# Kernel tuning notes

Hardware: AMD Instinct MI355X
Metric: run time of the kernel (lower is better)

The kernel has to match this reference:

```python
import jax, jax.numpy as jnp
import numpy as np

N = 50000      # nodes
E = 600000     # edges
F_IN = 128     # num_node_features
H = 128        # hidden_channels
C = 10         # num_classes
G = 128        # graphs in batch


def setup_inputs() -> dict:
    key = jax.random.key(0)
    ks = jax.random.split(key, 12)
    x = jax.random.normal(ks[0], (N, F_IN), dtype=jnp.float32)
    edge_index = jax.random.randint(ks[1], (2, E), 0, N, dtype=jnp.int64)
    batch = jnp.sort(jax.random.randint(ks[2], (N,), 0, G, dtype=jnp.int64))
    s = 0.05
    return {
        "x": x,
        "W1": jax.random.normal(ks[3], (F_IN, H), jnp.float32) * s,
        "b1": jnp.zeros((H,), jnp.float32),
        "W2": jax.random.normal(ks[4], (H, H), jnp.float32) * s,
        "b2": jnp.zeros((H,), jnp.float32),
        "W3": jax.random.normal(ks[5], (H, H), jnp.float32) * s,
        "b3": jnp.zeros((H,), jnp.float32),
        "Wl": jax.random.normal(ks[6], (H, C), jnp.float32) * s,
        "bl": jnp.zeros((C,), jnp.float32),
        "edge_index": edge_index,
        "batch": batch,
    }


def _gcn_conv(h, W, b, src, dst, norm, n):
    # h: [N, din] -> linear (no bias), gather, scale, scatter-add, + bias
    h = h @ W                                  # [N, dout]
    msg = norm[:, None] * h[src]               # [E+N, dout]
    out = jax.ops.segment_sum(msg, dst, num_segments=n)
    return out + b


def reference(x, W1, b1, W2, b2, W3, b3, Wl, bl, edge_index, batch):
    n = x.shape[0]
    # add self-loops (PyG GCNConv default) and symmetric normalization
    loop = jnp.arange(n, dtype=edge_index.dtype)
    src = jnp.concatenate([edge_index[0], loop])   # [E+N]
    dst = jnp.concatenate([edge_index[1], loop])   # [E+N]
    deg = jax.ops.segment_sum(jnp.ones_like(dst, dtype=x.dtype), dst, num_segments=n)
    dinv = jnp.where(deg > 0, jax.lax.rsqrt(deg), 0.0)
    norm = dinv[src] * dinv[dst]                   # [E+N]

    h = jax.nn.relu(_gcn_conv(x, W1, b1, src, dst, norm, n))
    h = jax.nn.relu(_gcn_conv(h, W2, b2, src, dst, norm, n))
    h = jax.nn.relu(_gcn_conv(h, W3, b3, src, dst, norm, n))

    # global mean pool over graph ids
    sums = jax.ops.segment_sum(h, batch, num_segments=G)           # [G, H]
    cnts = jax.ops.segment_sum(jnp.ones((n,), h.dtype), batch, num_segments=G)
    pooled = sums / jnp.maximum(cnts, 1.0)[:, None]

    # dropout is identity at inference; final linear classifier
    return pooled @ Wl + bl                                        # [G, C]
```

## Files before the change

kernel.cpp:

```cpp
#include <hip/hip_runtime.h>

#define HID 128
#define CLS 10
#define RCAP 64

typedef short short8 __attribute__((ext_vector_type(8)));
typedef float f32x4 __attribute__((ext_vector_type(4)));

__device__ __forceinline__ unsigned short f2bf(float f) {
  union { float f; unsigned u; } v; v.f = f;
  unsigned u = v.u;
  return (unsigned short)((u + 0x7FFFu + ((u >> 16) & 1u)) >> 16);
}
__device__ __forceinline__ float bf_lo(unsigned p) { return __uint_as_float(p << 16); }
__device__ __forceinline__ float bf_hi(unsigned p) { return __uint_as_float(p & 0xFFFF0000u); }


__global__ __launch_bounds__(256) void zero_wt(int* __restrict__ degi, int n, int nbN,
                                               float* __restrict__ pooled, int gh,
                                               const float* __restrict__ W1,
                                               const float* __restrict__ W2,
                                               const float* __restrict__ W3,
                                               unsigned short* __restrict__ Wt,
                                               unsigned short* __restrict__ TbZeroRow) {
  int b = blockIdx.x;
  if (b < nbN) {
    int i = b * 256 + threadIdx.x;
    if (i < n) degi[i] = 0;
    if (i < gh) pooled[i] = 0.f;
    if (b == 0 && threadIdx.x < 16) {
      uint4 z; z.x = z.y = z.z = z.w = 0u;
      *(uint4*)&TbZeroRow[threadIdx.x * 8] = z;
    }
    return;
  }
  int wb = b - nbN;
  int mat = wb >> 4;
  int part = wb & 15;
  const float* W = (mat == 0) ? W1 : (mat == 1) ? W2 : W3;
  unsigned short* o = Wt + (size_t)mat * HID * HID;
  int base = part * (HID * HID / 16);
  for (int r = 0; r < HID * HID / 16; r += 256) {
    int idx = base + r + threadIdx.x;
    int k = idx >> 7, nn = idx & 127;
    o[nn * HID + k] = f2bf(W[idx]);
  }
}

__global__ __launch_bounds__(256) void degree_fill(const int* __restrict__ src,
                                                   const int* __restrict__ dst,
                                                   int* __restrict__ degi,
                                                   int* __restrict__ col_src, int E) {
  int e = blockIdx.x * 256 + threadIdx.x;
  if (e >= E) return;
  int d = dst[e];
  int slot = atomicAdd(&degi[d], 1);
  if (slot < RCAP) col_src[(size_t)d * RCAP + slot] = src[e];
}


#define WTP 136

__global__ __launch_bounds__(256) void gemm_mfma(const void* __restrict__ Aptr,
                                                 int a_fp32,
                                                 const unsigned short* __restrict__ Wt,
                                                 const int* __restrict__ degi,
                                                 unsigned short* __restrict__ Tb,
                                                 int* __restrict__ pad_col,
                                                 int nrows) {
  __shared__ unsigned short sW[HID][WTP];
  int tid = threadIdx.x;
  int wave = tid >> 6, lane = tid & 63;
  int m_lo = lane & 15, quad = lane >> 4;
  int row0 = blockIdx.x * 128;
  int rbase = row0 + wave * 32;

  uint4 araw[2][4];
#pragma unroll
  for (int tr = 0; tr < 2; ++tr) {
    int grow = rbase + tr * 16 + m_lo;
    int gr = (grow < nrows) ? grow : (nrows - 1);
    if (a_fp32) {
      const float* Arow = (const float*)Aptr + (size_t)gr * HID;
#pragma unroll
      for (int kb = 0; kb < 4; ++kb) {
        float4 f0 = *(const float4*)&Arow[kb * 32 + quad * 8];
        float4 f1 = *(const float4*)&Arow[kb * 32 + quad * 8 + 4];
        uint4 u;
        u.x = (unsigned)f2bf(f0.x) | ((unsigned)f2bf(f0.y) << 16);
        u.y = (unsigned)f2bf(f0.z) | ((unsigned)f2bf(f0.w) << 16);
        u.z = (unsigned)f2bf(f1.x) | ((unsigned)f2bf(f1.y) << 16);
        u.w = (unsigned)f2bf(f1.z) | ((unsigned)f2bf(f1.w) << 16);
        araw[tr][kb] = u;
      }
    } else {
      const uint4* Arow = (const uint4*)((const unsigned*)Aptr + (size_t)gr * 64);
#pragma unroll
      for (int kb = 0; kb < 4; ++kb) araw[tr][kb] = Arow[kb * 4 + quad];
    }
  }

  const uint4* Wt4 = (const uint4*)Wt;
#pragma unroll
  for (int i = 0; i < 8; ++i) {
    int idx = i * 256 + tid;
    *(uint4*)&sW[idx >> 4][(idx & 15) * 8] = Wt4[idx];
  }
  __syncthreads();

  f32x4 acc[2][8];
#pragma unroll
  for (int tr = 0; tr < 2; ++tr)
#pragma unroll
    for (int tc = 0; tc < 8; ++tc) acc[tr][tc] = (f32x4)(0.f);

#pragma unroll
  for (int kb = 0; kb < 4; ++kb) {
    short8 b[8];
#pragma unroll
    for (int tc = 0; tc < 8; ++tc) {
      union { uint4 u; short8 s; } cv;
      cv.u = *(const uint4*)&sW[tc * 16 + m_lo][kb * 32 + quad * 8];
      b[tc] = cv.s;
    }
#pragma unroll
    for (int tr = 0; tr < 2; ++tr) {
      union { uint4 u; short8 s; } av;
      av.u = araw[tr][kb];
#pragma unroll
      for (int tc = 0; tc < 8; ++tc)
        acc[tr][tc] = __builtin_amdgcn_mfma_f32_16x16x32_bf16(av.s, b[tc], acc[tr][tc], 0, 0, 0);
    }
  }

#pragma unroll
  for (int tr = 0; tr < 2; ++tr) {
#pragma unroll
    for (int r = 0; r < 4; ++r) {
      int grow = rbase + tr * 16 + quad * 4 + r;
      if (grow < nrows) {
        int dgv = degi[grow];
        float s = rsqrtf((float)dgv + 1.0f);
        unsigned short* orow = &Tb[(size_t)grow * HID];
#pragma unroll
        for (int tc = 0; tc < 8; ++tc)
          orow[tc * 16 + m_lo] = f2bf(s * acc[tr][tc][r]);
        if (pad_col && m_lo == 0) {
          int d = dgv < RCAP ? dgv : RCAP;
          int dp = (d + 3) & ~3;
          for (int sl = d; sl < dp; ++sl)
            pad_col[(size_t)grow * RCAP + sl] = nrows;
        }
      }
    }
  }
}


__device__ __forceinline__ void agg_node(const unsigned* __restrict__ Tb2,
                                         const int* __restrict__ degi,
                                         const int* __restrict__ col_src,
                                         const float* __restrict__ bias,
                                         int node, int l4, float a[8]) {
  uint4 sv = *(const uint4*)&Tb2[(size_t)node * 64 + l4 * 4];
  a[0] = bf_lo(sv.x); a[1] = bf_hi(sv.x); a[2] = bf_lo(sv.y); a[3] = bf_hi(sv.y);
  a[4] = bf_lo(sv.z); a[5] = bf_hi(sv.z); a[6] = bf_lo(sv.w); a[7] = bf_hi(sv.w);
  int deg = degi[node];
  int dc = deg < RCAP ? deg : RCAP;
  int dp = (dc + 3) & ~3;
  const int* row = &col_src[(size_t)node * RCAP];
  int j = 0;
  for (; j + 8 <= dp; j += 8) {
    int idx[8];
#pragma unroll
    for (int u = 0; u < 8; ++u) idx[u] = row[j + u];
    uint4 v[8];
#pragma unroll
    for (int u = 0; u < 8; ++u) v[u] = *(const uint4*)&Tb2[(size_t)idx[u] * 64 + l4 * 4];
#pragma unroll
    for (int u = 0; u < 8; ++u) {
      a[0] += bf_lo(v[u].x); a[1] += bf_hi(v[u].x);
      a[2] += bf_lo(v[u].y); a[3] += bf_hi(v[u].y);
      a[4] += bf_lo(v[u].z); a[5] += bf_hi(v[u].z);
      a[6] += bf_lo(v[u].w); a[7] += bf_hi(v[u].w);
    }
  }
  if (j < dp) {
    int idx[4];
#pragma unroll
    for (int u = 0; u < 4; ++u) idx[u] = row[j + u];
    uint4 v[4];
#pragma unroll
    for (int u = 0; u < 4; ++u) v[u] = *(const uint4*)&Tb2[(size_t)idx[u] * 64 + l4 * 4];
#pragma unroll
    for (int u = 0; u < 4; ++u) {
      a[0] += bf_lo(v[u].x); a[1] += bf_hi(v[u].x);
      a[2] += bf_lo(v[u].y); a[3] += bf_hi(v[u].y);
      a[4] += bf_lo(v[u].z); a[5] += bf_hi(v[u].z);
      a[6] += bf_lo(v[u].w); a[7] += bf_hi(v[u].w);
    }
  }
  float di = rsqrtf((float)deg + 1.0f);
  float4 bs0 = *(const float4*)&bias[l4 * 8];
  float4 bs1 = *(const float4*)&bias[l4 * 8 + 4];
  a[0] = fmaxf(di * a[0] + bs0.x, 0.f);
  a[1] = fmaxf(di * a[1] + bs0.y, 0.f);
  a[2] = fmaxf(di * a[2] + bs0.z, 0.f);
  a[3] = fmaxf(di * a[3] + bs0.w, 0.f);
  a[4] = fmaxf(di * a[4] + bs1.x, 0.f);
  a[5] = fmaxf(di * a[5] + bs1.y, 0.f);
  a[6] = fmaxf(di * a[6] + bs1.z, 0.f);
  a[7] = fmaxf(di * a[7] + bs1.w, 0.f);
}

__global__ __launch_bounds__(256) void aggregate(const unsigned* __restrict__ Tb2,
                                                 const int* __restrict__ degi,
                                                 const int* __restrict__ col_src,
                                                 const float* __restrict__ bias,
                                                 unsigned* __restrict__ Hb, int n) {
  int w = (blockIdx.x * 256 + threadIdx.x) >> 6;
  int lane = threadIdx.x & 63;
  int sub = lane >> 4;
  int l4 = lane & 15;
  int node = w * 4 + sub;
  if (node >= n) return;
  float a[8];
  agg_node(Tb2, degi, col_src, bias, node, l4, a);
  uint4 o;
  o.x = (unsigned)f2bf(a[0]) | ((unsigned)f2bf(a[1]) << 16);
  o.y = (unsigned)f2bf(a[2]) | ((unsigned)f2bf(a[3]) << 16);
  o.z = (unsigned)f2bf(a[4]) | ((unsigned)f2bf(a[5]) << 16);
  o.w = (unsigned)f2bf(a[6]) | ((unsigned)f2bf(a[7]) << 16);
  *(uint4*)&Hb[(size_t)node * 64 + l4 * 4] = o;
}

#define SPP 132

__global__ __launch_bounds__(256) void aggregate_pool(const unsigned* __restrict__ Tb2,
                                                      const int* __restrict__ degi,
                                                      const int* __restrict__ col_src,
                                                      const float* __restrict__ bias,
                                                      const int* __restrict__ batch,
                                                      float* __restrict__ pooled, int n) {
  __shared__ float sP[16][SPP];
  int tid = threadIdx.x;
  int wave = tid >> 6, lane = tid & 63;
  int sub = lane >> 4;
  int l4 = lane & 15;
  int base = blockIdx.x * 16;
  int nl = wave * 4 + sub;
  int node = base + nl;
  bool active = (node < n);

  float a[8] = {0.f, 0.f, 0.f, 0.f, 0.f, 0.f, 0.f, 0.f};
  if (active) agg_node(Tb2, degi, col_src, bias, node, l4, a);
  *(float4*)&sP[nl][l4 * 8] = make_float4(a[0], a[1], a[2], a[3]);
  *(float4*)&sP[nl][l4 * 8 + 4] = make_float4(a[4], a[5], a[6], a[7]);
  __syncthreads();

  if (tid < HID) {
    int g = -1;
    float acc = 0.f;
    for (int i = 0; i < 16; ++i) {
      int nd = base + i;
      if (nd >= n) break;
      int bi = batch[nd];
      if (bi != g) {
        if (g >= 0) atomicAdd(&pooled[g * HID + tid], acc);
        acc = 0.f;
        g = bi;
      }
      acc += sP[i][tid];
    }
    if (g >= 0) atomicAdd(&pooled[g * HID + tid], acc);
  }
}

__global__ __launch_bounds__(128) void classify_k(const float* __restrict__ pooled,
                                                  const int* __restrict__ batch,
                                                  const float* __restrict__ Wl,
                                                  const float* __restrict__ bl,
                                                  float* __restrict__ out, int n) {
  int g = blockIdx.x;
  int t = threadIdx.x;
  int lo = 0, hi = n;
  while (lo < hi) { int mid = (lo + hi) >> 1; if (batch[mid] < g) lo = mid + 1; else hi = mid; }
  int s = lo;
  hi = n;
  while (lo < hi) { int mid = (lo + hi) >> 1; if (batch[mid] < g + 1) lo = mid + 1; else hi = mid; }
  float c = fmaxf((float)(lo - s), 1.0f);
  __shared__ float p[HID];
  p[t] = pooled[g * HID + t] / c;
  __syncthreads();
  if (t < CLS) {
    float o = bl[t];
    for (int j = 0; j < HID; ++j) o += p[j] * Wl[j * CLS + t];
    out[g * CLS + t] = o;
  }
}


extern "C" void kernel_launch(void* const* d_in, const int* in_sizes, int n_in,
                              void* d_out, int out_size, void* d_ws, size_t ws_size,
                              hipStream_t stream) {
  const float* x  = (const float*)d_in[0];
  const float* W1 = (const float*)d_in[1];
  const float* b1 = (const float*)d_in[2];
  const float* W2 = (const float*)d_in[3];
  const float* b2 = (const float*)d_in[4];
  const float* W3 = (const float*)d_in[5];
  const float* b3 = (const float*)d_in[6];
  const float* Wl = (const float*)d_in[7];
  const float* bl = (const float*)d_in[8];
  const int* edge_index = (const int*)d_in[9];
  const int* batch = (const int*)d_in[10];

  const int N = in_sizes[10];
  const int E = in_sizes[9] / 2;
  const int G = out_size / CLS;
  const int* src = edge_index;
  const int* dst = edge_index + E;

  uintptr_t p = (uintptr_t)d_ws;
  auto take = [&](size_t bytes) -> void* {
    void* r = (void*)p;
    p += (bytes + 255) & ~(size_t)255;
    return r;
  };
  int*      degi      = (int*)take((size_t)N * 4);
  int*      col_src   = (int*)take((size_t)N * RCAP * 4);
  unsigned short* WtA = (unsigned short*)take((size_t)3 * HID * HID * 2);
  unsigned short* bufTb = (unsigned short*)take((size_t)(N + 1) * HID * 2);
  unsigned* bufHb     = (unsigned*)take((size_t)N * 64 * 4);
  float*    pooled    = (float*)take((size_t)G * HID * 4);

  int nbN = (N + 255) / 256;
  int nbE = (E + 255) / 256;

  zero_wt<<<nbN + 48, 256, 0, stream>>>(degi, N, nbN, pooled, G * HID, W1, W2, W3, WtA,
                                        bufTb + (size_t)N * HID);
  degree_fill<<<nbE, 256, 0, stream>>>(src, dst, degi, col_src, E);

  int gemmBlocks = (N + 127) / 128;
  int waves = (N + 3) / 4;
  int aggBlocks = (waves + 3) / 4;

  gemm_mfma<<<gemmBlocks, 256, 0, stream>>>(x, 1, WtA, degi, bufTb, col_src, N);
  aggregate<<<aggBlocks, 256, 0, stream>>>((unsigned*)bufTb, degi, col_src, b1, bufHb, N);
  gemm_mfma<<<gemmBlocks, 256, 0, stream>>>(bufHb, 0, WtA + (size_t)HID * HID, degi, bufTb,
                                            nullptr, N);
  aggregate<<<aggBlocks, 256, 0, stream>>>((unsigned*)bufTb, degi, col_src, b2, bufHb, N);
  gemm_mfma<<<gemmBlocks, 256, 0, stream>>>(bufHb, 0, WtA + (size_t)2 * HID * HID, degi, bufTb,
                                            nullptr, N);
  aggregate_pool<<<(N + 15) / 16, 256, 0, stream>>>((unsigned*)bufTb, degi, col_src, b3,
                                                    batch, pooled, N);
  classify_k<<<G, 128, 0, stream>>>(pooled, batch, Wl, bl, (float*)d_out, N);
}
```

Measured before the change: 247.3 us.

## Bucket neighbor lists by source-index range and aggregate four nodes per thread

Neighbor lists are split into four buckets by source node index range, each with its own count, so the gathers for one bucket touch a narrower part of the feature table and should hit cache better. Aggregation now processes four nodes per 16-lane group and interleaves the gathers of two nodes so more loads are in flight. Outputs use nontemporal stores, and the pooling kernel works on 64 nodes per block. The trade-offs are more padding slots, a per-bucket cap of 24 that could drop edges for skewed graphs, and more registers per thread.

```diff
diff --git a/kernel.cpp b/kernel.cpp
--- a/kernel.cpp
+++ b/kernel.cpp
@@ -2,7 +2,9 @@
 
 #define HID 128
 #define CLS 10
-#define RCAP 64
+#define NW 4
+#define BCAP 24
+#define NSTR (NW * BCAP)
 
 typedef short short8 __attribute__((ext_vector_type(8)));
 typedef float f32x4 __attribute__((ext_vector_type(4)));
@@ -16,7 +18,7 @@
 __device__ __forceinline__ float bf_hi(unsigned p) { return __uint_as_float(p & 0xFFFF0000u); }
 
 
-__global__ __launch_bounds__(256) void zero_wt(int* __restrict__ degi, int n, int nbN,
+__global__ __launch_bounds__(256) void zero_wt(int* __restrict__ degw, int n, int nbN,
                                                float* __restrict__ pooled, int gh,
                                                const float* __restrict__ W1,
                                                const float* __restrict__ W2,
@@ -26,7 +28,7 @@
   int b = blockIdx.x;
   if (b < nbN) {
     int i = b * 256 + threadIdx.x;
-    if (i < n) degi[i] = 0;
+    if (i < n) { int4 z4; z4.x = z4.y = z4.z = z4.w = 0; *(int4*)&degw[(size_t)i * 4] = z4; }
     if (i < gh) pooled[i] = 0.f;
     if (b == 0 && threadIdx.x < 16) {
       uint4 z; z.x = z.y = z.z = z.w = 0u;
@@ -49,13 +51,17 @@
 
 __global__ __launch_bounds__(256) void degree_fill(const int* __restrict__ src,
                                                    const int* __restrict__ dst,
-                                                   int* __restrict__ degi,
-                                                   int* __restrict__ col_src, int E) {
+                                                   int* __restrict__ degw,
+                                                   int* __restrict__ col_src, int E,
+                                                   float wscale) {
   int e = blockIdx.x * 256 + threadIdx.x;
   if (e >= E) return;
+  int s = src[e];
   int d = dst[e];
-  int slot = atomicAdd(&degi[d], 1);
-  if (slot < RCAP) col_src[(size_t)d * RCAP + slot] = src[e];
+  int w = (int)((float)s * wscale);
+  if (w > NW - 1) w = NW - 1;
+  int slot = atomicAdd(&degw[(size_t)d * 4 + w], 1);
+  if (slot < BCAP) col_src[(size_t)d * NSTR + w * BCAP + slot] = s;
 }
 
 
@@ -64,7 +70,7 @@
 __global__ __launch_bounds__(256) void gemm_mfma(const void* __restrict__ Aptr,
                                                  int a_fp32,
                                                  const unsigned short* __restrict__ Wt,
-                                                 const int* __restrict__ degi,
+                                                 const int* __restrict__ degw,
                                                  unsigned short* __restrict__ Tb,
                                                  int* __restrict__ pad_col,
                                                  int nrows) {
@@ -139,17 +145,22 @@
     for (int r = 0; r < 4; ++r) {
       int grow = rbase + tr * 16 + quad * 4 + r;
       if (grow < nrows) {
-        int dgv = degi[grow];
+        int4 cwv = *(const int4*)&degw[(size_t)grow * 4];
+        int dgv = cwv.x + cwv.y + cwv.z + cwv.w;
         float s = rsqrtf((float)dgv + 1.0f);
         unsigned short* orow = &Tb[(size_t)grow * HID];
 #pragma unroll
         for (int tc = 0; tc < 8; ++tc)
           orow[tc * 16 + m_lo] = f2bf(s * acc[tr][tc][r]);
         if (pad_col && m_lo == 0) {
-          int d = dgv < RCAP ? dgv : RCAP;
-          int dp = (d + 3) & ~3;
-          for (int sl = d; sl < dp; ++sl)
-            pad_col[(size_t)grow * RCAP + sl] = nrows;
+#pragma unroll
+          for (int w = 0; w < NW; ++w) {
+            int cc = (w == 0) ? cwv.x : (w == 1) ? cwv.y : (w == 2) ? cwv.z : cwv.w;
+            int d = cc < BCAP ? cc : BCAP;
+            int dp = (d + 3) & ~3;
+            for (int sl = d; sl < dp; ++sl)
+              pad_col[(size_t)grow * NSTR + w * BCAP + sl] = nrows;
+          }
         }
       }
     }
@@ -157,122 +168,180 @@
 }
 
 
-__device__ __forceinline__ void agg_node(const unsigned* __restrict__ Tb2,
-                                         const int* __restrict__ degi,
+__device__ __forceinline__ void accum_row(float a[8], uint4 v) {
+  a[0] += bf_lo(v.x); a[1] += bf_hi(v.x);
+  a[2] += bf_lo(v.y); a[3] += bf_hi(v.y);
+  a[4] += bf_lo(v.z); a[5] += bf_hi(v.z);
+  a[6] += bf_lo(v.w); a[7] += bf_hi(v.w);
+}
+
+__device__ __forceinline__ uint4 tb_row(const unsigned* __restrict__ Tb2, int idx, int l4) {
+  return *(const uint4*)&Tb2[(size_t)idx * 64 + l4 * 4];
+}
+
+__device__ __forceinline__ int cw_get(int4 v, int w) {
+  return (w == 0) ? v.x : (w == 1) ? v.y : (w == 2) ? v.z : v.w;
+}
+
+__device__ __forceinline__ void agg_quad(const unsigned* __restrict__ Tb2,
                                          const int* __restrict__ col_src,
-                                         const float* __restrict__ bias,
-                                         int node, int l4, float a[8]) {
-  uint4 sv = *(const uint4*)&Tb2[(size_t)node * 64 + l4 * 4];
-  a[0] = bf_lo(sv.x); a[1] = bf_hi(sv.x); a[2] = bf_lo(sv.y); a[3] = bf_hi(sv.y);
-  a[4] = bf_lo(sv.z); a[5] = bf_hi(sv.z); a[6] = bf_lo(sv.w); a[7] = bf_hi(sv.w);
-  int deg = degi[node];
-  int dc = deg < RCAP ? deg : RCAP;
-  int dp = (dc + 3) & ~3;
-  const int* row = &col_src[(size_t)node * RCAP];
-  int j = 0;
-  for (; j + 8 <= dp; j += 8) {
-    int idx[8];
-#pragma unroll
-    for (int u = 0; u < 8; ++u) idx[u] = row[j + u];
-    uint4 v[8];
-#pragma unroll
-    for (int u = 0; u < 8; ++u) v[u] = *(const uint4*)&Tb2[(size_t)idx[u] * 64 + l4 * 4];
-#pragma unroll
-    for (int u = 0; u < 8; ++u) {
-      a[0] += bf_lo(v[u].x); a[1] += bf_hi(v[u].x);
-      a[2] += bf_lo(v[u].y); a[3] += bf_hi(v[u].y);
-      a[4] += bf_lo(v[u].z); a[5] += bf_hi(v[u].z);
-      a[6] += bf_lo(v[u].w); a[7] += bf_hi(v[u].w);
-    }
-  }
-  if (j < dp) {
-    int idx[4];
-#pragma unroll
-    for (int u = 0; u < 4; ++u) idx[u] = row[j + u];
-    uint4 v[4];
-#pragma unroll
-    for (int u = 0; u < 4; ++u) v[u] = *(const uint4*)&Tb2[(size_t)idx[u] * 64 + l4 * 4];
-#pragma unroll
-    for (int u = 0; u < 4; ++u) {
-      a[0] += bf_lo(v[u].x); a[1] += bf_hi(v[u].x);
-      a[2] += bf_lo(v[u].y); a[3] += bf_hi(v[u].y);
-      a[4] += bf_lo(v[u].z); a[5] += bf_hi(v[u].z);
-      a[6] += bf_lo(v[u].w); a[7] += bf_hi(v[u].w);
-    }
-  }
-  float di = rsqrtf((float)deg + 1.0f);
+                                         const int4 cw[4], const int nd[4], int l4,
+                                         int nzero, float acc[4][8]) {
+#pragma unroll
+  for (int c = 0; c < 4; ++c) {
+    uint4 sv = tb_row(Tb2, nd[c], l4);
+    acc[c][0] = bf_lo(sv.x); acc[c][1] = bf_hi(sv.x);
+    acc[c][2] = bf_lo(sv.y); acc[c][3] = bf_hi(sv.y);
+    acc[c][4] = bf_lo(sv.z); acc[c][5] = bf_hi(sv.z);
+    acc[c][6] = bf_lo(sv.w); acc[c][7] = bf_hi(sv.w);
+  }
+#pragma unroll
+  for (int w = 0; w < NW; ++w) {
+#pragma unroll
+    for (int cp = 0; cp < 2; ++cp) {
+      const int c0 = cp * 2, c1 = cp * 2 + 1;
+      int n0 = cw_get(cw[c0], w); n0 = n0 < BCAP ? n0 : BCAP;
+      int n1 = cw_get(cw[c1], w); n1 = n1 < BCAP ? n1 : BCAP;
+      int dp0 = (n0 + 3) & ~3, dp1 = (n1 + 3) & ~3;
+      const int* r0 = &col_src[(size_t)nd[c0] * NSTR + w * BCAP];
+      const int* r1 = &col_src[(size_t)nd[c1] * NSTR + w * BCAP];
+      int4 i0 = (dp0 > 0) ? *(const int4*)r0 : make_int4(nzero, nzero, nzero, nzero);
+      int4 i1 = (dp1 > 0) ? *(const int4*)r1 : make_int4(nzero, nzero, nzero, nzero);
+      uint4 v0[4], v1[4];
+      v0[0] = tb_row(Tb2, i0.x, l4); v0[1] = tb_row(Tb2, i0.y, l4);
+      v0[2] = tb_row(Tb2, i0.z, l4); v0[3] = tb_row(Tb2, i0.w, l4);
+      v1[0] = tb_row(Tb2, i1.x, l4); v1[1] = tb_row(Tb2, i1.y, l4);
+      v1[2] = tb_row(Tb2, i1.z, l4); v1[3] = tb_row(Tb2, i1.w, l4);
+#pragma unroll
+      for (int u = 0; u < 4; ++u) accum_row(acc[c0], v0[u]);
+#pragma unroll
+      for (int u = 0; u < 4; ++u) accum_row(acc[c1], v1[u]);
+      for (int j = 4; j < dp0; j += 4) {
+        int4 ii = *(const int4*)(r0 + j);
+        uint4 a0 = tb_row(Tb2, ii.x, l4), a1 = tb_row(Tb2, ii.y, l4);
+        uint4 a2 = tb_row(Tb2, ii.z, l4), a3 = tb_row(Tb2, ii.w, l4);
+        accum_row(acc[c0], a0); accum_row(acc[c0], a1);
+        accum_row(acc[c0], a2); accum_row(acc[c0], a3);
+      }
+      for (int j = 4; j < dp1; j += 4) {
+        int4 ii = *(const int4*)(r1 + j);
+        uint4 a0 = tb_row(Tb2, ii.x, l4), a1 = tb_row(Tb2, ii.y, l4);
+        uint4 a2 = tb_row(Tb2, ii.z, l4), a3 = tb_row(Tb2, ii.w, l4);
+        accum_row(acc[c1], a0); accum_row(acc[c1], a1);
+        accum_row(acc[c1], a2); accum_row(acc[c1], a3);
+      }
+    }
+  }
+}
+
+__global__ __launch_bounds__(256) void aggregate(const unsigned* __restrict__ Tb2,
+                                                 const int* __restrict__ degw,
+                                                 const int* __restrict__ col_src,
+                                                 const float* __restrict__ bias,
+                                                 unsigned* __restrict__ Hb, int n, int nzero) {
+  int tid = threadIdx.x;
+  int g = tid >> 4, l4 = tid & 15;
+  int base = blockIdx.x * 64 + g * 4;
+  int nd[4]; int4 cw[4];
+#pragma unroll
+  for (int c = 0; c < 4; ++c) {
+    int node = base + c;
+    nd[c] = node < n ? node : (n - 1);
+    cw[c] = *(const int4*)&degw[(size_t)nd[c] * 4];
+  }
+  float acc[4][8];
+  agg_quad(Tb2, col_src, cw, nd, l4, nzero, acc);
+
   float4 bs0 = *(const float4*)&bias[l4 * 8];
   float4 bs1 = *(const float4*)&bias[l4 * 8 + 4];
-  a[0] = fmaxf(di * a[0] + bs0.x, 0.f);
-  a[1] = fmaxf(di * a[1] + bs0.y, 0.f);
-  a[2] = fmaxf(di * a[2] + bs0.z, 0.f);
-  a[3] = fmaxf(di * a[3] + bs0.w, 0.f);
-  a[4] = fmaxf(di * a[4] + bs1.x, 0.f);
-  a[5] = fmaxf(di * a[5] + bs1.y, 0.f);
-  a[6] = fmaxf(di * a[6] + bs1.z, 0.f);
-  a[7] = fmaxf(di * a[7] + bs1.w, 0.f);
-}
-
-__global__ __launch_bounds__(256) void aggregate(const unsigned* __restrict__ Tb2,
-                                                 const int* __restrict__ degi,
-                                                 const int* __restrict__ col_src,
-                                                 const float* __restrict__ bias,
-                                                 unsigned* __restrict__ Hb, int n) {
-  int w = (blockIdx.x * 256 + threadIdx.x) >> 6;
-  int lane = threadIdx.x & 63;
-  int sub = lane >> 4;
-  int l4 = lane & 15;
-  int node = w * 4 + sub;
-  if (node >= n) return;
-  float a[8];
-  agg_node(Tb2, degi, col_src, bias, node, l4, a);
-  uint4 o;
-  o.x = (unsigned)f2bf(a[0]) | ((unsigned)f2bf(a[1]) << 16);
-  o.y = (unsigned)f2bf(a[2]) | ((unsigned)f2bf(a[3]) << 16);
-  o.z = (unsigned)f2bf(a[4]) | ((unsigned)f2bf(a[5]) << 16);
-  o.w = (unsigned)f2bf(a[6]) | ((unsigned)f2bf(a[7]) << 16);
-  *(uint4*)&Hb[(size_t)node * 64 + l4 * 4] = o;
+#pragma unroll
+  for (int c = 0; c < 4; ++c) {
+    int node = base + c;
+    if (node < n) {
+      int deg = cw[c].x + cw[c].y + cw[c].z + cw[c].w;
+      float di = rsqrtf((float)deg + 1.0f);
+      float o0 = fmaxf(di * acc[c][0] + bs0.x, 0.f);
+      float o1 = fmaxf(di * acc[c][1] + bs0.y, 0.f);
+      float o2 = fmaxf(di * acc[c][2] + bs0.z, 0.f);
+      float o3 = fmaxf(di * acc[c][3] + bs0.w, 0.f);
+      float o4 = fmaxf(di * acc[c][4] + bs1.x, 0.f);
+      float o5 = fmaxf(di * acc[c][5] + bs1.y, 0.f);
+      float o6 = fmaxf(di * acc[c][6] + bs1.z, 0.f);
+      float o7 = fmaxf(di * acc[c][7] + bs1.w, 0.f);
+      union { uint4 u4; unsigned long long ll[2]; } o;
+      o.u4.x = (unsigned)f2bf(o0) | ((unsigned)f2bf(o1) << 16);
+      o.u4.y = (unsigned)f2bf(o2) | ((unsigned)f2bf(o3) << 16);
+      o.u4.z = (unsigned)f2bf(o4) | ((unsigned)f2bf(o5) << 16);
+      o.u4.w = (unsigned)f2bf(o6) | ((unsigned)f2bf(o7) << 16);
+      unsigned long long* dst = (unsigned long long*)&Hb[(size_t)node * 64 + l4 * 4];
+      __builtin_nontemporal_store(o.ll[0], dst);
+      __builtin_nontemporal_store(o.ll[1], dst + 1);
+    }
+  }
 }
 
 #define SPP 132
 
 __global__ __launch_bounds__(256) void aggregate_pool(const unsigned* __restrict__ Tb2,
-                                                      const int* __restrict__ degi,
+                                                      const int* __restrict__ degw,
                                                       const int* __restrict__ col_src,
                                                       const float* __restrict__ bias,
                                                       const int* __restrict__ batch,
-                                                      float* __restrict__ pooled, int n) {
-  __shared__ float sP[16][SPP];
+                                                      float* __restrict__ pooled, int n,
+                                                      int nzero) {
+  __shared__ float sP[64][SPP];
   int tid = threadIdx.x;
-  int wave = tid >> 6, lane = tid & 63;
-  int sub = lane >> 4;
-  int l4 = lane & 15;
-  int base = blockIdx.x * 16;
-  int nl = wave * 4 + sub;
-  int node = base + nl;
-  bool active = (node < n);
-
-  float a[8] = {0.f, 0.f, 0.f, 0.f, 0.f, 0.f, 0.f, 0.f};
-  if (active) agg_node(Tb2, degi, col_src, bias, node, l4, a);
-  *(float4*)&sP[nl][l4 * 8] = make_float4(a[0], a[1], a[2], a[3]);
-  *(float4*)&sP[nl][l4 * 8 + 4] = make_float4(a[4], a[5], a[6], a[7]);
+  int g = tid >> 4, l4 = tid & 15;
+  int base = blockIdx.x * 64;
+  int nb = base + g * 4;
+  int nd[4]; int4 cw[4];
+#pragma unroll
+  for (int c = 0; c < 4; ++c) {
+    int node = nb + c;
+    nd[c] = node < n ? node : (n - 1);
+    cw[c] = *(const int4*)&degw[(size_t)nd[c] * 4];
+  }
+  float acc[4][8];
+  agg_quad(Tb2, col_src, cw, nd, l4, nzero, acc);
+
+  float4 bs0 = *(const float4*)&bias[l4 * 8];
+  float4 bs1 = *(const float4*)&bias[l4 * 8 + 4];
+#pragma unroll
+  for (int c = 0; c < 4; ++c) {
+    int deg = cw[c].x + cw[c].y + cw[c].z + cw[c].w;
+    float di = rsqrtf((float)deg + 1.0f);
+    float o0 = fmaxf(di * acc[c][0] + bs0.x, 0.f);
+    float o1 = fmaxf(di * acc[c][1] + bs0.y, 0.f);
+    float o2 = fmaxf(di * acc[c][2] + bs0.z, 0.f);
+    float o3 = fmaxf(di * acc[c][3] + bs0.w, 0.f);
+    float o4 = fmaxf(di * acc[c][4] + bs1.x, 0.f);
+    float o5 = fmaxf(di * acc[c][5] + bs1.y, 0.f);
+    float o6 = fmaxf(di * acc[c][6] + bs1.z, 0.f);
+    float o7 = fmaxf(di * acc[c][7] + bs1.w, 0.f);
+    int nl = g * 4 + c;
+    *(float4*)&sP[nl][l4 * 8] = make_float4(o0, o1, o2, o3);
+    *(float4*)&sP[nl][l4 * 8 + 4] = make_float4(o4, o5, o6, o7);
+  }
   __syncthreads();
 
-  if (tid < HID) {
-    int g = -1;
-    float acc = 0.f;
-    for (int i = 0; i < 16; ++i) {
-      int nd = base + i;
-      if (nd >= n) break;
-      int bi = batch[nd];
-      if (bi != g) {
-        if (g >= 0) atomicAdd(&pooled[g * HID + tid], acc);
-        acc = 0.f;
-        g = bi;
+  {
+    int f = tid & 127;
+    int h = tid >> 7;
+    int i0 = h * 32, i1 = i0 + 32;
+    int gq = -1;
+    float accv = 0.f;
+    for (int i = i0; i < i1; ++i) {
+      int ndl = base + i;
+      if (ndl >= n) break;
+      int bi = batch[ndl];
+      if (bi != gq) {
+        if (gq >= 0) atomicAdd(&pooled[gq * HID + f], accv);
+        accv = 0.f;
+        gq = bi;
       }
-      acc += sP[i][tid];
-    }
-    if (g >= 0) atomicAdd(&pooled[g * HID + tid], acc);
+      accv += sP[i][f];
+    }
+    if (gq >= 0) atomicAdd(&pooled[gq * HID + f], accv);
   }
 }
 
@@ -327,8 +396,8 @@
     p += (bytes + 255) & ~(size_t)255;
     return r;
   };
-  int*      degi      = (int*)take((size_t)N * 4);
-  int*      col_src   = (int*)take((size_t)N * RCAP * 4);
+  int*      degw      = (int*)take((size_t)N * 4 * 4);
+  int*      col_src   = (int*)take((size_t)N * NSTR * 4);
   unsigned short* WtA = (unsigned short*)take((size_t)3 * HID * HID * 2);
   unsigned short* bufTb = (unsigned short*)take((size_t)(N + 1) * HID * 2);
   unsigned* bufHb     = (unsigned*)take((size_t)N * 64 * 4);
@@ -336,23 +405,23 @@
 
   int nbN = (N + 255) / 256;
   int nbE = (E + 255) / 256;
-
-  zero_wt<<<nbN + 48, 256, 0, stream>>>(degi, N, nbN, pooled, G * HID, W1, W2, W3, WtA,
+  float wscale = (float)NW / (float)N;
+
+  zero_wt<<<nbN + 48, 256, 0, stream>>>(degw, N, nbN, pooled, G * HID, W1, W2, W3, WtA,
                                         bufTb + (size_t)N * HID);
-  degree_fill<<<nbE, 256, 0, stream>>>(src, dst, degi, col_src, E);
+  degree_fill<<<nbE, 256, 0, stream>>>(src, dst, degw, col_src, E, wscale);
 
   int gemmBlocks = (N + 127) / 128;
-  int waves = (N + 3) / 4;
-  int aggBlocks = (waves + 3) / 4;
-
-  gemm_mfma<<<gemmBlocks, 256, 0, stream>>>(x, 1, WtA, degi, bufTb, col_src, N);
-  aggregate<<<aggBlocks, 256, 0, stream>>>((unsigned*)bufTb, degi, col_src, b1, bufHb, N);
-  gemm_mfma<<<gemmBlocks, 256, 0, stream>>>(bufHb, 0, WtA + (size_t)HID * HID, degi, bufTb,
+  int aggBlocks = (N + 63) / 64;
+
+  gemm_mfma<<<gemmBlocks, 256, 0, stream>>>(x, 1, WtA, degw, bufTb, col_src, N);
+  aggregate<<<aggBlocks, 256, 0, stream>>>((unsigned*)bufTb, degw, col_src, b1, bufHb, N, N);
+  gemm_mfma<<<gemmBlocks, 256, 0, stream>>>(bufHb, 0, WtA + (size_t)HID * HID, degw, bufTb,
                                             nullptr, N);
-  aggregate<<<aggBlocks, 256, 0, stream>>>((unsigned*)bufTb, degi, col_src, b2, bufHb, N);
-  gemm_mfma<<<gemmBlocks, 256, 0, stream>>>(bufHb, 0, WtA + (size_t)2 * HID * HID, degi, bufTb,
+  aggregate<<<aggBlocks, 256, 0, stream>>>((unsigned*)bufTb, degw, col_src, b2, bufHb, N, N);
+  gemm_mfma<<<gemmBlocks, 256, 0, stream>>>(bufHb, 0, WtA + (size_t)2 * HID * HID, degw, bufTb,
                                             nullptr, N);
-  aggregate_pool<<<(N + 15) / 16, 256, 0, stream>>>((unsigned*)bufTb, degi, col_src, b3,
-                                                    batch, pooled, N);
+  aggregate_pool<<<aggBlocks, 256, 0, stream>>>((unsigned*)bufTb, degw, col_src, b3,
+                                                batch, pooled, N, N);
   classify_k<<<G, 128, 0, stream>>>(pooled, batch, Wl, bl, (float*)d_out, N);
 }
```

Measured after the change: 289.8 us. +17.2%, slower.

## Fuse neighbor aggregation with next layer GEMM via shared-memory tile

Applied to the files above, without the earlier changes.

Replaces the separate aggregate and gemm_mfma launches for layers 2 and 3 with a single kernel. Each 16-node block aggregates neighbors into shared memory as bf16, then multiplies by the next weight matrix using MFMA and writes the degree-scaled result. The intermediate H buffer round-trip and two launches are removed, and two ping-pong T buffers with zero pad rows are used instead. The cost is that every small block reloads the full 128x128 weight tile into LDS, and higher LDS use may reduce occupancy.

```diff
diff --git a/kernel.cpp b/kernel.cpp
--- a/kernel.cpp
+++ b/kernel.cpp
@@ -22,7 +22,8 @@
                                                const float* __restrict__ W2,
                                                const float* __restrict__ W3,
                                                unsigned short* __restrict__ Wt,
-                                               unsigned short* __restrict__ TbZeroRow) {
+                                               unsigned short* __restrict__ TzA,
+                                               unsigned short* __restrict__ TzB) {
   int b = blockIdx.x;
   if (b < nbN) {
     int i = b * 256 + threadIdx.x;
@@ -30,7 +31,8 @@
     if (i < gh) pooled[i] = 0.f;
     if (b == 0 && threadIdx.x < 16) {
       uint4 z; z.x = z.y = z.z = z.w = 0u;
-      *(uint4*)&TbZeroRow[threadIdx.x * 8] = z;
+      *(uint4*)&TzA[threadIdx.x * 8] = z;
+      *(uint4*)&TzB[threadIdx.x * 8] = z;
     }
     return;
   }
@@ -61,8 +63,7 @@
 
 #define WTP 136
 
-__global__ __launch_bounds__(256) void gemm_mfma(const void* __restrict__ Aptr,
-                                                 int a_fp32,
+__global__ __launch_bounds__(256) void gemm_mfma(const float* __restrict__ Aptr,
                                                  const unsigned short* __restrict__ Wt,
                                                  const int* __restrict__ degi,
                                                  unsigned short* __restrict__ Tb,
@@ -80,23 +81,17 @@
   for (int tr = 0; tr < 2; ++tr) {
     int grow = rbase + tr * 16 + m_lo;
     int gr = (grow < nrows) ? grow : (nrows - 1);
-    if (a_fp32) {
-      const float* Arow = (const float*)Aptr + (size_t)gr * HID;
-#pragma unroll
-      for (int kb = 0; kb < 4; ++kb) {
-        float4 f0 = *(const float4*)&Arow[kb * 32 + quad * 8];
-        float4 f1 = *(const float4*)&Arow[kb * 32 + quad * 8 + 4];
-        uint4 u;
-        u.x = (unsigned)f2bf(f0.x) | ((unsigned)f2bf(f0.y) << 16);
-        u.y = (unsigned)f2bf(f0.z) | ((unsigned)f2bf(f0.w) << 16);
-        u.z = (unsigned)f2bf(f1.x) | ((unsigned)f2bf(f1.y) << 16);
-        u.w = (unsigned)f2bf(f1.z) | ((unsigned)f2bf(f1.w) << 16);
-        araw[tr][kb] = u;
-      }
-    } else {
-      const uint4* Arow = (const uint4*)((const unsigned*)Aptr + (size_t)gr * 64);
-#pragma unroll
-      for (int kb = 0; kb < 4; ++kb) araw[tr][kb] = Arow[kb * 4 + quad];
+    const float* Arow = Aptr + (size_t)gr * HID;
+#pragma unroll
+    for (int kb = 0; kb < 4; ++kb) {
+      float4 f0 = *(const float4*)&Arow[kb * 32 + quad * 8];
+      float4 f1 = *(const float4*)&Arow[kb * 32 + quad * 8 + 4];
+      uint4 u;
+      u.x = (unsigned)f2bf(f0.x) | ((unsigned)f2bf(f0.y) << 16);
+      u.y = (unsigned)f2bf(f0.z) | ((unsigned)f2bf(f0.w) << 16);
+      u.z = (unsigned)f2bf(f1.x) | ((unsigned)f2bf(f1.y) << 16);
+      u.w = (unsigned)f2bf(f1.z) | ((unsigned)f2bf(f1.w) << 16);
+      araw[tr][kb] = u;
     }
   }
 
@@ -145,7 +140,7 @@
 #pragma unroll
         for (int tc = 0; tc < 8; ++tc)
           orow[tc * 16 + m_lo] = f2bf(s * acc[tr][tc][r]);
-        if (pad_col && m_lo == 0) {
+        if (m_lo == 0) {
           int d = dgv < RCAP ? dgv : RCAP;
           int dp = (d + 3) & ~3;
           for (int sl = d; sl < dp; ++sl)
@@ -213,25 +208,67 @@
   a[7] = fmaxf(di * a[7] + bs1.w, 0.f);
 }
 
-__global__ __launch_bounds__(256) void aggregate(const unsigned* __restrict__ Tb2,
-                                                 const int* __restrict__ degi,
-                                                 const int* __restrict__ col_src,
-                                                 const float* __restrict__ bias,
-                                                 unsigned* __restrict__ Hb, int n) {
-  int w = (blockIdx.x * 256 + threadIdx.x) >> 6;
-  int lane = threadIdx.x & 63;
-  int sub = lane >> 4;
-  int l4 = lane & 15;
-  int node = w * 4 + sub;
-  if (node >= n) return;
+
+__global__ __launch_bounds__(256, 4) void fused_agg_gemm(const unsigned* __restrict__ Tb_in,
+                                                         const int* __restrict__ degi,
+                                                         const int* __restrict__ col_src,
+                                                         const float* __restrict__ bias,
+                                                         const unsigned short* __restrict__ Wt,
+                                                         unsigned short* __restrict__ Tb_out,
+                                                         int n) {
+  __shared__ unsigned short sW[HID][WTP];
+  __shared__ unsigned short sH[16][WTP];
+  int tid = threadIdx.x;
+
+  const uint4* Wt4 = (const uint4*)Wt;
+#pragma unroll
+  for (int i = 0; i < 8; ++i) {
+    int idx = i * 256 + tid;
+    *(uint4*)&sW[idx >> 4][(idx & 15) * 8] = Wt4[idx];
+  }
+
+  int nl = tid >> 4, l4 = tid & 15;
+  int node = blockIdx.x * 16 + nl;
+  int nodec = node < n ? node : (n - 1);
   float a[8];
-  agg_node(Tb2, degi, col_src, bias, node, l4, a);
+  agg_node(Tb_in, degi, col_src, bias, nodec, l4, a);
   uint4 o;
   o.x = (unsigned)f2bf(a[0]) | ((unsigned)f2bf(a[1]) << 16);
   o.y = (unsigned)f2bf(a[2]) | ((unsigned)f2bf(a[3]) << 16);
   o.z = (unsigned)f2bf(a[4]) | ((unsigned)f2bf(a[5]) << 16);
   o.w = (unsigned)f2bf(a[6]) | ((unsigned)f2bf(a[7]) << 16);
-  *(uint4*)&Hb[(size_t)node * 64 + l4 * 4] = o;
+  *(uint4*)&sH[nl][l4 * 8] = o;
+  __syncthreads();
+
+  int wid = tid >> 6, lane = tid & 63;
+  int m_lo = lane & 15, quad = lane >> 4;
+  f32x4 acc[2];
+  acc[0] = (f32x4)(0.f); acc[1] = (f32x4)(0.f);
+#pragma unroll
+  for (int kb = 0; kb < 4; ++kb) {
+    union { uint4 u; short8 s; } av;
+    av.u = *(const uint4*)&sH[m_lo][kb * 32 + quad * 8];
+#pragma unroll
+    for (int t = 0; t < 2; ++t) {
+      int tc = wid * 2 + t;
+      union { uint4 u; short8 s; } bv;
+      bv.u = *(const uint4*)&sW[tc * 16 + m_lo][kb * 32 + quad * 8];
+      acc[t] = __builtin_amdgcn_mfma_f32_16x16x32_bf16(av.s, bv.s, acc[t], 0, 0, 0);
+    }
+  }
+#pragma unroll
+  for (int r = 0; r < 4; ++r) {
+    int grow = blockIdx.x * 16 + quad * 4 + r;
+    if (grow < n) {
+      float s = rsqrtf((float)degi[grow] + 1.0f);
+      unsigned short* orow = &Tb_out[(size_t)grow * HID];
+#pragma unroll
+      for (int t = 0; t < 2; ++t) {
+        int tc = wid * 2 + t;
+        orow[tc * 16 + m_lo] = f2bf(s * acc[t][r]);
+      }
+    }
+  }
 }
 
 #define SPP 132
@@ -330,29 +367,26 @@
   int*      degi      = (int*)take((size_t)N * 4);
   int*      col_src   = (int*)take((size_t)N * RCAP * 4);
   unsigned short* WtA = (unsigned short*)take((size_t)3 * HID * HID * 2);
+  unsigned short* bufTa = (unsigned short*)take((size_t)(N + 1) * HID * 2);
   unsigned short* bufTb = (unsigned short*)take((size_t)(N + 1) * HID * 2);
-  unsigned* bufHb     = (unsigned*)take((size_t)N * 64 * 4);
   float*    pooled    = (float*)take((size_t)G * HID * 4);
 
   int nbN = (N + 255) / 256;
   int nbE = (E + 255) / 256;
 
   zero_wt<<<nbN + 48, 256, 0, stream>>>(degi, N, nbN, pooled, G * HID, W1, W2, W3, WtA,
-                                        bufTb + (size_t)N * HID);
+                                        bufTa + (size_t)N * HID, bufTb + (size_t)N * HID);
   degree_fill<<<nbE, 256, 0, stream>>>(src, dst, degi, col_src, E);
 
   int gemmBlocks = (N + 127) / 128;
-  int waves = (N + 3) / 4;
-  int aggBlocks = (waves + 3) / 4;
-
-  gemm_mfma<<<gemmBlocks, 256, 0, stream>>>(x, 1, WtA, degi, bufTb, col_src, N);
-  aggregate<<<aggBlocks, 256, 0, stream>>>((unsigned*)bufTb, degi, col_src, b1, bufHb, N);
-  gemm_mfma<<<gemmBlocks, 256, 0, stream>>>(bufHb, 0, WtA + (size_t)HID * HID, degi, bufTb,
-                                            nullptr, N);
-  aggregate<<<aggBlocks, 256, 0, stream>>>((unsigned*)bufTb, degi, col_src, b2, bufHb, N);
-  gemm_mfma<<<gemmBlocks, 256, 0, stream>>>(bufHb, 0, WtA + (size_t)2 * HID * HID, degi, bufTb,
-                                            nullptr, N);
-  aggregate_pool<<<(N + 15) / 16, 256, 0, stream>>>((unsigned*)bufTb, degi, col_src, b3,
-                                                    batch, pooled, N);
+  int aggBlocks = (N + 15) / 16;
+
+  gemm_mfma<<<gemmBlocks, 256, 0, stream>>>(x, WtA, degi, bufTa, col_src, N);
+  fused_agg_gemm<<<aggBlocks, 256, 0, stream>>>((unsigned*)bufTa, degi, col_src, b1,
+                                                WtA + (size_t)HID * HID, bufTb, N);
+  fused_agg_gemm<<<aggBlocks, 256, 0, stream>>>((unsigned*)bufTb, degi, col_src, b2,
+                                                WtA + (size_t)2 * HID * HID, bufTa, N);
+  aggregate_pool<<<aggBlocks, 256, 0, stream>>>((unsigned*)bufTa, degi, col_src, b3,
+                                                batch, pooled, N);
   classify_k<<<G, 128, 0, stream>>>(pooled, batch, Wl, bl, (float*)d_out, N);
 }
```

Result: faster. 227.4 us (-8.1%).
